# Kernel optimization log

Measured on AMD Instinct MI355X. Metric: run time of the kernel, lower is better.

The kernel has to match this reference:

```python
import jax, jax.numpy as jnp
import numpy as np

N_PDE = 4096
SENSOR_RANGE = 0.08
WINDOW = int(SENSOR_RANGE * N_PDE)   # 327
HALF = WINDOW // 2                   # 163
RESIZE_LEN = 20
FREQS = jnp.array([1.0, 2.0, 4.0, 8.0], dtype=jnp.float32)
EPS = 1e-6  # flax GroupNorm default epsilon
U_MAX, V_MAX = 40.0, 1.0
N_AGENTS = 262144


def setup_inputs() -> dict:
    key = jax.random.key(0)
    ks = jax.random.split(key, 16)

    def w(k, shape):
        fan_in = shape[0]
        return (jax.random.normal(k, shape, jnp.float32) / np.float32(np.sqrt(fan_in)))

    return {
        "z_curr": jax.random.normal(ks[0], (N_PDE,), jnp.float32),
        "z_target": jax.random.normal(ks[1], (N_PDE,), jnp.float32),
        "xi_curr": jax.random.uniform(ks[2], (N_AGENTS,), jnp.float32),
        # branch net (features=[256,256]), each layer: Dense + GroupNorm(1 group) + tanh
        "bW0": w(ks[3], (2 * RESIZE_LEN, 256)), "bb0": jnp.zeros((256,), jnp.float32),
        "bs0": jnp.ones((256,), jnp.float32), "bB0": jnp.zeros((256,), jnp.float32),
        "bW1": w(ks[4], (256, 256)), "bb1": jnp.zeros((256,), jnp.float32),
        "bs1": jnp.ones((256,), jnp.float32), "bB1": jnp.zeros((256,), jnp.float32),
        # trunk net: 8 -> 32 -> 32
        "tW0": w(ks[5], (8, 32)), "tb0": jnp.zeros((32,), jnp.float32),
        "tW1": w(ks[6], (32, 32)), "tb1": jnp.zeros((32,), jnp.float32),
        # combined head: (256+32) -> 32, then two 32 -> 1 heads
        "cW": w(ks[7], (256 + 32, 32)), "cb": jnp.zeros((32,), jnp.float32),
        "uW": w(ks[8], (32, 1)), "ub": jnp.zeros((1,), jnp.float32),
        "vW": w(ks[9], (32, 1)), "vb": jnp.zeros((1,), jnp.float32),
    }


def _local_obs(padded_error, xi):
    # per-agent dynamic slice + finite-difference gradient + bilinear resize
    center = (xi * (N_PDE - 1)).astype(jnp.int32) + HALF
    start = center - HALF
    p_err = jax.lax.dynamic_slice(padded_error, (start,), (WINDOW,))
    p_grad = jnp.gradient(p_err)
    p_err = jax.image.resize(p_err, (RESIZE_LEN,), method='bilinear')
    p_grad = jax.image.resize(p_grad, (RESIZE_LEN,), method='bilinear')
    return jnp.concatenate([p_err, p_grad])  # [40]


def _groupnorm1(x, scale, bias):
    # GroupNorm(num_groups=1) applied per-sample over the feature axis
    mu = jnp.mean(x, axis=-1, keepdims=True)
    var = jnp.var(x, axis=-1, keepdims=True)
    return (x - mu) * jax.lax.rsqrt(var + EPS) * scale + bias


def reference(z_curr, z_target, xi_curr,
              bW0, bb0, bs0, bB0, bW1, bb1, bs1, bB1,
              tW0, tb0, tW1, tb1, cW, cb, uW, ub, vW, vb):
    error = z_curr - z_target
    padded = jnp.pad(error, (HALF, HALF), mode='edge')  # [N_PDE + 2*HALF]

    patches = jax.vmap(lambda xi: _local_obs(padded, xi))(xi_curr)  # [A, 40]

    # branch net
    h = jnp.tanh(_groupnorm1(patches @ bW0 + bb0, bs0, bB0))  # [A, 256]
    h = jnp.tanh(_groupnorm1(h @ bW1 + bb1, bs1, bB1))        # [A, 256]

    # trunk net
    angle = xi_curr[:, None] * FREQS * jnp.pi                 # [A, 4]
    enc = jnp.concatenate([jnp.sin(angle), jnp.cos(angle)], axis=-1)  # [A, 8]
    enc = jnp.tanh(enc @ tW0 + tb0)
    enc = jnp.tanh(enc @ tW1 + tb1)                           # [A, 32]

    combined = jnp.concatenate([h, enc], axis=-1)             # [A, 288]
    x = jnp.tanh(combined @ cW + cb)                          # [A, 32]
    u_raw = (x @ uW + ub).squeeze(-1)
    v_raw = (x @ vW + vb).squeeze(-1)
    return (U_MAX * jnp.tanh(u_raw), V_MAX * jnp.tanh(v_raw))
```

## Files before the change

### kernel.cpp

```cpp
#include <hip/hip_runtime.h>
#include <hip/hip_fp16.h>

#define NP      4096
#define WINDOW  327
#define HALF    163
#define RL      20
#define NA      262144
#define GN_EPS  1e-6f
#define R       8
#define NBLK    (NP / R)

__device__ __forceinline__ float tanh_fast(float x) {
  float e = __expf(2.0f * x);
  return 1.0f - 2.0f / (e + 1.0f);
}

__device__ __forceinline__ void wave_sum64_2(float& a, float& b) {
#pragma unroll
  for (int m = 1; m < 64; m <<= 1) {
    a += __shfl_xor(a, m, 64);
    b += __shfl_xor(b, m, 64);
  }
}

#define L_ESP   0
#define L_OBS   336
#define L_HBUF  656
#define L_HCL   2736
#define L_TOTF  3024

__global__ __launch_bounds__(512, 4) void dc_table(
    const float* __restrict__ zc,  const float* __restrict__ zt,
    const float* __restrict__ bW0, const float* __restrict__ bb0,
    const float* __restrict__ bs0, const float* __restrict__ bB0,
    const float* __restrict__ bW1, const float* __restrict__ bb1,
    const float* __restrict__ bs1, const float* __restrict__ bB1,
    const float* __restrict__ tW0, const float* __restrict__ tb0,
    const float* __restrict__ tW1, const float* __restrict__ tb1,
    const float* __restrict__ cW,  const float* __restrict__ cb,
    const float* __restrict__ uW,  const float* __restrict__ ub,
    const float* __restrict__ vW,  const float* __restrict__ vb,
    float* __restrict__ tbl)
{
  __shared__ __align__(16) float  smf[L_TOTF];
  __shared__ __align__(16) __half2 part[8 * 8 * 128];
  float* espan = smf + L_ESP;
  float* obsT  = smf + L_OBS;
  float* hbuf  = smf + L_HBUF;
  float* hcL   = smf + L_HCL;

  const int tid = threadIdx.x;
  const int w   = tid >> 6;
  const int l   = tid & 63;
  const int s0  = blockIdx.x * R;

  for (int t = tid; t < WINDOW + R - 1; t += 512) {
    int c = s0 - HALF + t;
    c = c < 0 ? 0 : (c > NP - 1 ? NP - 1 : c);
    espan[t] = zc[c] - zt[c];
  }
  __syncthreads();

  {
    const float INV  = (float)WINDOW / (float)RL;
    const float RINV = (float)RL / (float)WINDOW;
    for (int task = tid; task < R * 2 * RL; task += 512) {
      int q = task % (2 * RL);
      int r = task / (2 * RL);
      int qq = (q < RL) ? q : q - RL;
      float xs = ((float)qq + 0.5f) * INV - 0.5f;
      int jlo = (int)ceilf(xs - INV);  if (jlo < 0) jlo = 0;
      int jhi = (int)floorf(xs + INV); if (jhi > WINDOW - 1) jhi = WINDOW - 1;
      const float* p = espan + r;
      float wsum = 0.0f, acc = 0.0f;
      for (int j = jlo; j <= jhi; ++j) {
        float wq = 1.0f - fabsf(xs - (float)j) * RINV;
        float v;
        if (q < RL) {
          v = p[j];
        } else {
          v = (j == 0) ? (p[1] - p[0]) :
              (j == WINDOW - 1) ? (p[WINDOW - 1] - p[WINDOW - 2]) :
              0.5f * (p[j + 1] - p[j - 1]);
        }
        wsum += wq;
        acc  += wq * v;
      }
      obsT[q * 8 + r] = acc / wsum;
    }
  }
  __syncthreads();

  float acc[R][4];

#pragma unroll
  for (int r = 0; r < R; ++r) { acc[r][0]=0.f; acc[r][1]=0.f; acc[r][2]=0.f; acc[r][3]=0.f; }
  for (int kk = 0; kk < 5; ++kk) {
    int k = w * 5 + kk;
    float4 wt = *(const float4*)&bW0[k * 256 + 4 * l];
    float4 o0 = *(const float4*)&obsT[k * 8];
    float4 o1 = *(const float4*)&obsT[k * 8 + 4];
    const float wv[4] = {wt.x, wt.y, wt.z, wt.w};
    const float ov[8] = {o0.x, o0.y, o0.z, o0.w, o1.x, o1.y, o1.z, o1.w};
#pragma unroll
    for (int r = 0; r < R; ++r)
#pragma unroll
      for (int j = 0; j < 4; ++j) acc[r][j] = fmaf(ov[r], wv[j], acc[r][j]);
  }
#pragma unroll
  for (int r = 0; r < R; ++r) {
    part[w * 1024 + r * 128 + 2 * l]     = __float22half2_rn(make_float2(acc[r][0], acc[r][1]));
    part[w * 1024 + r * 128 + 2 * l + 1] = __float22half2_rn(make_float2(acc[r][2], acc[r][3]));
  }
  __syncthreads();

  {
    const int rr = w, g = l;
    float4 b = *(const float4*)&bb0[4 * g];
    float v0 = b.x, v1 = b.y, v2 = b.z, v3 = b.w;
#pragma unroll
    for (int w2 = 0; w2 < 8; ++w2) {
      float2 p0 = __half22float2(part[w2 * 1024 + rr * 128 + 2 * g]);
      float2 p1 = __half22float2(part[w2 * 1024 + rr * 128 + 2 * g + 1]);
      v0 += p0.x; v1 += p0.y; v2 += p1.x; v3 += p1.y;
    }
    float s = v0 + v1 + v2 + v3;
    float q = v0*v0 + v1*v1 + v2*v2 + v3*v3;
    wave_sum64_2(s, q);
    float mu  = s * (1.0f / 256.0f);
    float var = fmaxf(q * (1.0f / 256.0f) - mu * mu, 0.0f);
    float rv  = rsqrtf(var + GN_EPS);
    float4 sc = *(const float4*)&bs0[4 * g];
    float4 sh = *(const float4*)&bB0[4 * g];
    float4 h;
    h.x = tanh_fast((v0 - mu) * rv * sc.x + sh.x);
    h.y = tanh_fast((v1 - mu) * rv * sc.y + sh.y);
    h.z = tanh_fast((v2 - mu) * rv * sc.z + sh.z);
    h.w = tanh_fast((v3 - mu) * rv * sc.w + sh.w);
    *(float4*)&hbuf[rr * 260 + 4 * g] = h;
  }
  __syncthreads();

#pragma unroll
  for (int r = 0; r < R; ++r) { acc[r][0]=0.f; acc[r][1]=0.f; acc[r][2]=0.f; acc[r][3]=0.f; }
  for (int kk = 0; kk < 32; kk += 4) {
    int k0 = w * 32 + kk;
    float4 wt0 = *(const float4*)&bW1[(k0    ) * 256 + 4 * l];
    float4 wt1 = *(const float4*)&bW1[(k0 + 1) * 256 + 4 * l];
    float4 wt2 = *(const float4*)&bW1[(k0 + 2) * 256 + 4 * l];
    float4 wt3 = *(const float4*)&bW1[(k0 + 3) * 256 + 4 * l];
#pragma unroll
    for (int r = 0; r < R; ++r) {
      float4 hv = *(const float4*)&hbuf[r * 260 + k0];
      acc[r][0] = fmaf(hv.x, wt0.x, acc[r][0]); acc[r][1] = fmaf(hv.x, wt0.y, acc[r][1]);
      acc[r][2] = fmaf(hv.x, wt0.z, acc[r][2]); acc[r][3] = fmaf(hv.x, wt0.w, acc[r][3]);
      acc[r][0] = fmaf(hv.y, wt1.x, acc[r][0]); acc[r][1] = fmaf(hv.y, wt1.y, acc[r][1]);
      acc[r][2] = fmaf(hv.y, wt1.z, acc[r][2]); acc[r][3] = fmaf(hv.y, wt1.w, acc[r][3]);
      acc[r][0] = fmaf(hv.z, wt2.x, acc[r][0]); acc[r][1] = fmaf(hv.z, wt2.y, acc[r][1]);
      acc[r][2] = fmaf(hv.z, wt2.z, acc[r][2]); acc[r][3] = fmaf(hv.z, wt2.w, acc[r][3]);
      acc[r][0] = fmaf(hv.w, wt3.x, acc[r][0]); acc[r][1] = fmaf(hv.w, wt3.y, acc[r][1]);
      acc[r][2] = fmaf(hv.w, wt3.z, acc[r][2]); acc[r][3] = fmaf(hv.w, wt3.w, acc[r][3]);
    }
  }
  __syncthreads();
#pragma unroll
  for (int r = 0; r < R; ++r) {
    part[w * 1024 + r * 128 + 2 * l]     = __float22half2_rn(make_float2(acc[r][0], acc[r][1]));
    part[w * 1024 + r * 128 + 2 * l + 1] = __float22half2_rn(make_float2(acc[r][2], acc[r][3]));
  }
  __syncthreads();

  {
    const int rr = w, g = l;
    float4 b = *(const float4*)&bb1[4 * g];
    float v0 = b.x, v1 = b.y, v2 = b.z, v3 = b.w;
#pragma unroll
    for (int w2 = 0; w2 < 8; ++w2) {
      float2 p0 = __half22float2(part[w2 * 1024 + rr * 128 + 2 * g]);
      float2 p1 = __half22float2(part[w2 * 1024 + rr * 128 + 2 * g + 1]);
      v0 += p0.x; v1 += p0.y; v2 += p1.x; v3 += p1.y;
    }
    float s = v0 + v1 + v2 + v3;
    float q = v0*v0 + v1*v1 + v2*v2 + v3*v3;
    wave_sum64_2(s, q);
    float mu  = s * (1.0f / 256.0f);
    float var = fmaxf(q * (1.0f / 256.0f) - mu * mu, 0.0f);
    float rv  = rsqrtf(var + GN_EPS);
    float4 sc = *(const float4*)&bs1[4 * g];
    float4 sh = *(const float4*)&bB1[4 * g];
    float4 h;
    h.x = tanh_fast((v0 - mu) * rv * sc.x + sh.x);
    h.y = tanh_fast((v1 - mu) * rv * sc.y + sh.y);
    h.z = tanh_fast((v2 - mu) * rv * sc.z + sh.z);
    h.w = tanh_fast((v3 - mu) * rv * sc.w + sh.w);
    *(float4*)&hbuf[rr * 260 + 4 * g] = h;
  }
  __syncthreads();

  {
    int r = tid >> 6;
    int c = l >> 1, kh = l & 1;
    float ga = (kh == 0) ? cb[c] : 0.0f;
    int kbase = kh * 128;
#pragma unroll 4
    for (int k = 0; k < 128; k += 4) {
      float4 hv = *(const float4*)&hbuf[r * 260 + kbase + k];
      ga = fmaf(hv.x, cW[(kbase + k    ) * 32 + c], ga);
      ga = fmaf(hv.y, cW[(kbase + k + 1) * 32 + c], ga);
      ga = fmaf(hv.z, cW[(kbase + k + 2) * 32 + c], ga);
      ga = fmaf(hv.w, cW[(kbase + k + 3) * 32 + c], ga);
    }
    ga += __shfl_xor(ga, 1, 64);
    if (kh == 0) hcL[r * 36 + c] = ga;
  }
  __syncthreads();

  if (tid < 128) {
    int v = tid >> 3, sub = tid & 7;
    int r = v >> 1, e = v & 1;
    int jg = s0 + r + e;
    float xe = (float)jg * (1.0f / 4095.0f);
    float enc[8];
#pragma unroll
    for (int k = 0; k < 4; ++k) {
      float fr = (float)(1 << k);
      float a = (xe * fr) * 3.14159265358979f;
      enc[k]     = sinf(a);
      enc[k + 4] = cosf(a);
    }
    int base = (tid & 63) & ~7;

    float t0v[4];
#pragma unroll
    for (int i = 0; i < 4; ++i) {
      int f = 4 * sub + i;
      float a = tb0[f];
#pragma unroll
      for (int k = 0; k < 8; ++k) a = fmaf(enc[k], tW0[k * 32 + f], a);
      t0v[i] = tanh_fast(a);
    }

    float t1v[4];
#pragma unroll
    for (int i = 0; i < 4; ++i) t1v[i] = tb1[4 * sub + i];
#pragma unroll
    for (int j8 = 0; j8 < 8; ++j8) {
#pragma unroll
      for (int i2 = 0; i2 < 4; ++i2) {
        float tv = __shfl(t0v[i2], base + j8, 64);
        int k = 4 * j8 + i2;
#pragma unroll
        for (int i = 0; i < 4; ++i) t1v[i] = fmaf(tv, tW1[k * 32 + 4 * sub + i], t1v[i]);
      }
    }
#pragma unroll
    for (int i = 0; i < 4; ++i) t1v[i] = tanh_fast(t1v[i]);

    float xvv[4];
#pragma unroll
    for (int i = 0; i < 4; ++i) xvv[i] = hcL[r * 36 + 4 * sub + i];
#pragma unroll
    for (int j8 = 0; j8 < 8; ++j8) {
#pragma unroll
      for (int i2 = 0; i2 < 4; ++i2) {
        float tv = __shfl(t1v[i2], base + j8, 64);
        int k = 4 * j8 + i2;
#pragma unroll
        for (int i = 0; i < 4; ++i) xvv[i] = fmaf(tv, cW[(256 + k) * 32 + 4 * sub + i], xvv[i]);
      }
    }
#pragma unroll
    for (int i = 0; i < 4; ++i) xvv[i] = tanh_fast(xvv[i]);

    float up = 0.f, vp = 0.f;
#pragma unroll
    for (int i = 0; i < 4; ++i) {
      up = fmaf(xvv[i], uW[4 * sub + i], up);
      vp = fmaf(xvv[i], vW[4 * sub + i], vp);
    }
#pragma unroll
    for (int m = 1; m < 8; m <<= 1) {
      up += __shfl_xor(up, m, 64);
      vp += __shfl_xor(vp, m, 64);
    }
    if (sub == 0) {
      int s = s0 + r;
      tbl[4 * s + e]     = 40.0f * tanh_fast(up + ub[0]);
      tbl[4 * s + 2 + e] = tanh_fast(vp + vb[0]);
    }
  }
}

__global__ __launch_bounds__(256) void dc_agents(
    const float* __restrict__ xi_curr, const float4* __restrict__ tbl,
    float* __restrict__ out)
{
  int a = blockIdx.x * 256 + threadIdx.x;
  float xi = xi_curr[a];
  float p = xi * 4095.0f;
  int s = (int)p;
  s = s > 4095 ? 4095 : s;
  float t = p - (float)s;
  float4 tb = tbl[s];
  out[a]      = fmaf(t, tb.y - tb.x, tb.x);
  out[NA + a] = fmaf(t, tb.w - tb.z, tb.z);
}

extern "C" void kernel_launch(void* const* d_in, const int* in_sizes, int n_in,
                              void* d_out, int out_size, void* d_ws, size_t ws_size,
                              hipStream_t stream) {
  const float* zc  = (const float*)d_in[0];
  const float* zt  = (const float*)d_in[1];
  const float* xi  = (const float*)d_in[2];
  const float* bW0 = (const float*)d_in[3];
  const float* bb0 = (const float*)d_in[4];
  const float* bs0 = (const float*)d_in[5];
  const float* bB0 = (const float*)d_in[6];
  const float* bW1 = (const float*)d_in[7];
  const float* bb1 = (const float*)d_in[8];
  const float* bs1 = (const float*)d_in[9];
  const float* bB1 = (const float*)d_in[10];
  const float* tW0 = (const float*)d_in[11];
  const float* tb0 = (const float*)d_in[12];
  const float* tW1 = (const float*)d_in[13];
  const float* tb1 = (const float*)d_in[14];
  const float* cW  = (const float*)d_in[15];
  const float* cb  = (const float*)d_in[16];
  const float* uW  = (const float*)d_in[17];
  const float* ub  = (const float*)d_in[18];
  const float* vW  = (const float*)d_in[19];
  const float* vb  = (const float*)d_in[20];

  float* tbl = (float*)d_ws;
  float* out = (float*)d_out;

  dc_table<<<NBLK, 512, 0, stream>>>(zc, zt, bW0, bb0, bs0, bB0,
                                     bW1, bb1, bs1, bB1,
                                     tW0, tb0, tW1, tb1, cW, cb,
                                     uW, ub, vW, vb, tbl);
  dc_agents<<<NA / 256, 256, 0, stream>>>(xi, (const float4*)tbl, out);
}
```

Before: 136.6 us.

## Halve table block to 4 rows and 256 threads with fp32 partial sums

The table kernel now handles 4 sample positions per block with 4 waves instead of 8 positions with 8 waves. This doubles the grid size and gives each wave twice the K-range per layer. Partial sums across waves are now stored as fp32 float4 in shared memory instead of fp16 half2, which removes conversion instructions and the fp16 rounding. It also drops one barrier. In exchange, every block reloads the full bW0/bW1 weights for half as many rows, doubling weight traffic per output row, and the tail trunk stage uses only one wave.

```diff
diff --git a/kernel.cpp b/kernel.cpp
--- a/kernel.cpp
+++ b/kernel.cpp
@@ -1,5 +1,4 @@
 #include <hip/hip_runtime.h>
-#include <hip/hip_fp16.h>
 
 #define NP      4096
 #define WINDOW  327
@@ -7,7 +6,7 @@
 #define RL      20
 #define NA      262144
 #define GN_EPS  1e-6f
-#define R       8
+#define R       4
 #define NBLK    (NP / R)
 
 __device__ __forceinline__ float tanh_fast(float x) {
@@ -25,11 +24,12 @@
 
 #define L_ESP   0
 #define L_OBS   336
-#define L_HBUF  656
-#define L_HCL   2736
-#define L_TOTF  3024
-
-__global__ __launch_bounds__(512, 4) void dc_table(
+#define L_HBUF  496
+#define L_PART  1536
+#define L_HCL   5632
+#define L_TOT   5776
+
+__global__ __launch_bounds__(256, 4) void dc_table(
     const float* __restrict__ zc,  const float* __restrict__ zt,
     const float* __restrict__ bW0, const float* __restrict__ bb0,
     const float* __restrict__ bs0, const float* __restrict__ bB0,
@@ -42,19 +42,19 @@
     const float* __restrict__ vW,  const float* __restrict__ vb,
     float* __restrict__ tbl)
 {
-  __shared__ __align__(16) float  smf[L_TOTF];
-  __shared__ __align__(16) __half2 part[8 * 8 * 128];
-  float* espan = smf + L_ESP;
-  float* obsT  = smf + L_OBS;
-  float* hbuf  = smf + L_HBUF;
-  float* hcL   = smf + L_HCL;
+  __shared__ __align__(16) float sm[L_TOT];
+  float* espan = sm + L_ESP;
+  float* obsT  = sm + L_OBS;
+  float* hbuf  = sm + L_HBUF;
+  float* part  = sm + L_PART;
+  float* hcL   = sm + L_HCL;
 
   const int tid = threadIdx.x;
   const int w   = tid >> 6;
   const int l   = tid & 63;
   const int s0  = blockIdx.x * R;
 
-  for (int t = tid; t < WINDOW + R - 1; t += 512) {
+  for (int t = tid; t < WINDOW + R - 1; t += 256) {
     int c = s0 - HALF + t;
     c = c < 0 ? 0 : (c > NP - 1 ? NP - 1 : c);
     espan[t] = zc[c] - zt[c];
@@ -64,7 +64,7 @@
   {
     const float INV  = (float)WINDOW / (float)RL;
     const float RINV = (float)RL / (float)WINDOW;
-    for (int task = tid; task < R * 2 * RL; task += 512) {
+    for (int task = tid; task < R * 2 * RL; task += 256) {
       int q = task % (2 * RL);
       int r = task / (2 * RL);
       int qq = (q < RL) ? q : q - RL;
@@ -86,7 +86,7 @@
         wsum += wq;
         acc  += wq * v;
       }
-      obsT[q * 8 + r] = acc / wsum;
+      obsT[q * 4 + r] = acc / wsum;
     }
   }
   __syncthreads();
@@ -95,23 +95,21 @@
 
 #pragma unroll
   for (int r = 0; r < R; ++r) { acc[r][0]=0.f; acc[r][1]=0.f; acc[r][2]=0.f; acc[r][3]=0.f; }
-  for (int kk = 0; kk < 5; ++kk) {
-    int k = w * 5 + kk;
+#pragma unroll 2
+  for (int kk = 0; kk < 10; ++kk) {
+    int k = w * 10 + kk;
     float4 wt = *(const float4*)&bW0[k * 256 + 4 * l];
-    float4 o0 = *(const float4*)&obsT[k * 8];
-    float4 o1 = *(const float4*)&obsT[k * 8 + 4];
+    float4 ov = *(const float4*)&obsT[k * 4];
     const float wv[4] = {wt.x, wt.y, wt.z, wt.w};
-    const float ov[8] = {o0.x, o0.y, o0.z, o0.w, o1.x, o1.y, o1.z, o1.w};
+    const float os[4] = {ov.x, ov.y, ov.z, ov.w};
 #pragma unroll
     for (int r = 0; r < R; ++r)
 #pragma unroll
-      for (int j = 0; j < 4; ++j) acc[r][j] = fmaf(ov[r], wv[j], acc[r][j]);
-  }
-#pragma unroll
-  for (int r = 0; r < R; ++r) {
-    part[w * 1024 + r * 128 + 2 * l]     = __float22half2_rn(make_float2(acc[r][0], acc[r][1]));
-    part[w * 1024 + r * 128 + 2 * l + 1] = __float22half2_rn(make_float2(acc[r][2], acc[r][3]));
-  }
+      for (int j = 0; j < 4; ++j) acc[r][j] = fmaf(os[r], wv[j], acc[r][j]);
+  }
+#pragma unroll
+  for (int r = 0; r < R; ++r)
+    *(float4*)&part[w * 1024 + r * 256 + 4 * l] = make_float4(acc[r][0], acc[r][1], acc[r][2], acc[r][3]);
   __syncthreads();
 
   {
@@ -119,10 +117,9 @@
     float4 b = *(const float4*)&bb0[4 * g];
     float v0 = b.x, v1 = b.y, v2 = b.z, v3 = b.w;
 #pragma unroll
-    for (int w2 = 0; w2 < 8; ++w2) {
-      float2 p0 = __half22float2(part[w2 * 1024 + rr * 128 + 2 * g]);
-      float2 p1 = __half22float2(part[w2 * 1024 + rr * 128 + 2 * g + 1]);
-      v0 += p0.x; v1 += p0.y; v2 += p1.x; v3 += p1.y;
+    for (int w2 = 0; w2 < 4; ++w2) {
+      float4 p4 = *(const float4*)&part[w2 * 1024 + rr * 256 + 4 * g];
+      v0 += p4.x; v1 += p4.y; v2 += p4.z; v3 += p4.w;
     }
     float s = v0 + v1 + v2 + v3;
     float q = v0*v0 + v1*v1 + v2*v2 + v3*v3;
@@ -143,8 +140,9 @@
 
 #pragma unroll
   for (int r = 0; r < R; ++r) { acc[r][0]=0.f; acc[r][1]=0.f; acc[r][2]=0.f; acc[r][3]=0.f; }
-  for (int kk = 0; kk < 32; kk += 4) {
-    int k0 = w * 32 + kk;
+#pragma unroll 2
+  for (int kk = 0; kk < 64; kk += 4) {
+    int k0 = w * 64 + kk;
     float4 wt0 = *(const float4*)&bW1[(k0    ) * 256 + 4 * l];
     float4 wt1 = *(const float4*)&bW1[(k0 + 1) * 256 + 4 * l];
     float4 wt2 = *(const float4*)&bW1[(k0 + 2) * 256 + 4 * l];
@@ -162,12 +160,9 @@
       acc[r][2] = fmaf(hv.w, wt3.z, acc[r][2]); acc[r][3] = fmaf(hv.w, wt3.w, acc[r][3]);
     }
   }
-  __syncthreads();
-#pragma unroll
-  for (int r = 0; r < R; ++r) {
-    part[w * 1024 + r * 128 + 2 * l]     = __float22half2_rn(make_float2(acc[r][0], acc[r][1]));
-    part[w * 1024 + r * 128 + 2 * l + 1] = __float22half2_rn(make_float2(acc[r][2], acc[r][3]));
-  }
+#pragma unroll
+  for (int r = 0; r < R; ++r)
+    *(float4*)&part[w * 1024 + r * 256 + 4 * l] = make_float4(acc[r][0], acc[r][1], acc[r][2], acc[r][3]);
   __syncthreads();
 
   {
@@ -175,10 +170,9 @@
     float4 b = *(const float4*)&bb1[4 * g];
     float v0 = b.x, v1 = b.y, v2 = b.z, v3 = b.w;
 #pragma unroll
-    for (int w2 = 0; w2 < 8; ++w2) {
-      float2 p0 = __half22float2(part[w2 * 1024 + rr * 128 + 2 * g]);
-      float2 p1 = __half22float2(part[w2 * 1024 + rr * 128 + 2 * g + 1]);
-      v0 += p0.x; v1 += p0.y; v2 += p1.x; v3 += p1.y;
+    for (int w2 = 0; w2 < 4; ++w2) {
+      float4 p4 = *(const float4*)&part[w2 * 1024 + rr * 256 + 4 * g];
+      v0 += p4.x; v1 += p4.y; v2 += p4.z; v3 += p4.w;
     }
     float s = v0 + v1 + v2 + v3;
     float q = v0*v0 + v1*v1 + v2*v2 + v3*v3;
@@ -215,7 +209,7 @@
   }
   __syncthreads();
 
-  if (tid < 128) {
+  if (tid < 64) {
     int v = tid >> 3, sub = tid & 7;
     int r = v >> 1, e = v & 1;
     int jg = s0 + r + e;
@@ -228,7 +222,7 @@
       enc[k]     = sinf(a);
       enc[k + 4] = cosf(a);
     }
-    int base = (tid & 63) & ~7;
+    int base = tid & ~7;
 
     float t0v[4];
 #pragma unroll
@@ -334,7 +328,7 @@
   float* tbl = (float*)d_ws;
   float* out = (float*)d_out;
 
-  dc_table<<<NBLK, 512, 0, stream>>>(zc, zt, bW0, bb0, bs0, bB0,
+  dc_table<<<NBLK, 256, 0, stream>>>(zc, zt, bW0, bb0, bs0, bB0,
                                      bW1, bb1, bs1, bB1,
                                      tW0, tb0, tW1, tb1, cW, cb,
                                      uW, ub, vW, vb, tbl);
```

Result: faster. 133.7 us (-2.1%).
